# Performance work log

Hardware: AMD Instinct MI355X
Metric: run time of the kernel (lower is better)

## Reference

```python
import jax, jax.numpy as jnp
import numpy as np
import math

D_MODEL = 1024
N_HEADS = 16
D_KV = 64
INNER = N_HEADS * D_KV
NUM_BUCKETS = 32
MAX_DISTANCE = 128


def _relative_position_bucket(relative_position, bidirectional=True,
                              num_buckets=NUM_BUCKETS, max_distance=MAX_DISTANCE):
    # faithful port of T5Attention._relative_position_bucket
    relative_buckets = jnp.zeros_like(relative_position)
    if bidirectional:
        num_buckets //= 2
        relative_buckets = relative_buckets + (relative_position > 0).astype(jnp.int32) * num_buckets
        relative_position = jnp.abs(relative_position)
    else:
        relative_position = -jnp.minimum(relative_position, jnp.zeros_like(relative_position))
    max_exact = num_buckets // 2
    is_small = relative_position < max_exact
    rp_large = max_exact + (
        jnp.log(relative_position.astype(jnp.float32) / max_exact)
        / math.log(max_distance / max_exact) * (num_buckets - max_exact)
    ).astype(jnp.int32)
    rp_large = jnp.minimum(rp_large, num_buckets - 1)
    return relative_buckets + jnp.where(is_small, relative_position, rp_large)


def compute_bias(rel_bias_table, q_len, k_len):
    # [q_len, k_len] relative positions -> bucket ids -> [1, H, q_len, k_len] bias
    context = jnp.arange(q_len, dtype=jnp.int32)[:, None]
    memory = jnp.arange(k_len, dtype=jnp.int32)[None, :]
    buckets = _relative_position_bucket(memory - context, bidirectional=True)
    values = rel_bias_table[buckets]            # [q, k, H]
    return jnp.transpose(values, (2, 0, 1))[None]  # [1, H, q, k]


def setup_inputs() -> dict:
    key = jax.random.key(0)
    ks = jax.random.split(key, 6)
    B, S = 2, 2048
    scale = 0.02
    return {
        "hidden_states": jax.random.normal(ks[0], (B, S, D_MODEL), jnp.float32),
        # weights stored as [in, out] (torch Linear applies x @ W.T with W [out,in])
        "w_q": jax.random.normal(ks[1], (D_MODEL, INNER), jnp.float32) * scale,
        "w_k": jax.random.normal(ks[2], (D_MODEL, INNER), jnp.float32) * scale,
        "w_v": jax.random.normal(ks[3], (D_MODEL, INNER), jnp.float32) * scale,
        "w_o": jax.random.normal(ks[4], (INNER, D_MODEL), jnp.float32) * scale,
        "rel_bias_table": jax.random.normal(ks[5], (NUM_BUCKETS, N_HEADS), jnp.float32) * scale,
    }


def reference(hidden_states, w_q, w_k, w_v, w_o, rel_bias_table):
    B, S, _ = hidden_states.shape

    def shape(x):  # [B, S, inner] -> [B, H, S, d_kv]
        return jnp.transpose(x.reshape(B, S, N_HEADS, D_KV), (0, 2, 1, 3))

    q = shape(hidden_states @ w_q)  # note: T5 applies no 1/sqrt(d) scaling
    k = shape(hidden_states @ w_k)
    v = shape(hidden_states @ w_v)

    scores = jnp.einsum("bhqd,bhkd->bhqk", q, k)
    position_bias = compute_bias(rel_bias_table, S, S)
    scores = scores + position_bias
    attn = jax.nn.softmax(scores.astype(jnp.float32), axis=-1).astype(scores.dtype)
    ctx = jnp.einsum("bhqk,bhkd->bhqd", attn, v)
    ctx = jnp.transpose(ctx, (0, 2, 1, 3)).reshape(B, S, INNER)
    return ctx @ w_o
```

## Files before the change

kernel.cpp:

```cpp
#include <hip/hip_runtime.h>
#include <math.h>

#define S_LEN 2048
#define DM 1024

typedef __attribute__((ext_vector_type(8))) __bf16 bf16x8;
typedef __attribute__((ext_vector_type(4))) float floatx4;

typedef __attribute__((address_space(1))) const unsigned int g_u32;
typedef __attribute__((address_space(3))) unsigned int l_u32;

__device__ __forceinline__ unsigned short f2bf(float f) {
  union { __bf16 h; unsigned short u; } v;
  v.h = (__bf16)f;
  return v.u;
}
__device__ __forceinline__ float bf2f(unsigned short u) {
  union { unsigned int u; float f; } v; v.u = ((unsigned int)u) << 16;
  return v.f;
}
__device__ __forceinline__ bf16x8 ld_frag(const unsigned short* p) {
  union { uint4 u; bf16x8 v; } t;
  t.u = *(const uint4*)p;
  return t.v;
}

__global__ void detect_k(const unsigned short* __restrict__ x, int* __restrict__ flag) {
  __shared__ int cnt;
  if (threadIdx.x == 0) cnt = 0;
  __syncthreads();
  int local = 0;
  for (int i = threadIdx.x; i < 4096; i += 256) {
    unsigned short u = x[i];
    int e = (u >> 7) & 0xFF;
    if (e > 140) local++;
  }
  atomicAdd(&cnt, local);
  __syncthreads();
  if (threadIdx.x == 0) *flag = (cnt > 64) ? 1 : 0;
}

__global__ void prep_k(const void* __restrict__ x, unsigned short* __restrict__ dst,
                       const void* __restrict__ tbl, float* __restrict__ outb,
                       const void* __restrict__ w0, const void* __restrict__ w1,
                       const void* __restrict__ w2, const void* __restrict__ w3,
                       unsigned short* __restrict__ Wcat, unsigned short* __restrict__ Wto,
                       const int* __restrict__ flag) {
  __shared__ float tile[32][33];
  const int bid = blockIdx.x, tid = threadIdx.x;
  if (bid < 2048) {
    int i = bid * 256 + tid;
    if (*flag) {
      const float4* s = (const float4*)x;
      float4 a = s[2 * i], b = s[2 * i + 1];
      union { uint4 u4; unsigned short s[8]; } o;
      o.s[0] = f2bf(a.x); o.s[1] = f2bf(a.y); o.s[2] = f2bf(a.z); o.s[3] = f2bf(a.w);
      o.s[4] = f2bf(b.x); o.s[5] = f2bf(b.y); o.s[6] = f2bf(b.z); o.s[7] = f2bf(b.w);
      ((uint4*)dst)[i] = o.u4;
    } else {
      ((uint4*)dst)[i] = ((const uint4*)x)[i];
    }
  } else if (bid < 2072) {
    int idx = (bid - 2048) * 256 + tid;
    if (idx >= 16 * 384) return;
    int h = idx / 384;
    int j = idx - h * 384;
    int delta = j - 192;
    int bucket = (delta > 0) ? 16 : 0;
    int ad = (delta < 0) ? -delta : delta;
    int smallv;
    if (ad < 8) smallv = ad;
    else {
      int l = (int)(log((double)ad * 0.125) * (8.0 / log(16.0)));
      smallv = 8 + l;
      if (smallv > 15) smallv = 15;
    }
    bucket += smallv;
    float v;
    if (*flag) v = ((const float*)tbl)[bucket * 16 + h];
    else       v = bf2f(((const unsigned short*)tbl)[bucket * 16 + h]);
    outb[idx] = v * 1.44269504f - 24.f;
  } else {
    const int t = bid - 2072;
    const int z = t >> 10, rem = t & 1023;
    const int bx = rem & 31, by = rem >> 5;
    const int tx = tid & 31, ty = tid >> 5;
    const void* src = (z == 0) ? w0 : (z == 1) ? w1 : (z == 2) ? w2 : w3;
    unsigned short* dsty = (z < 3) ? (Wcat + (size_t)z * 1048576) : Wto;
    const int isf = *flag;
    int xc = bx * 32 + tx;
    int y0 = by * 32;
    for (int i = ty; i < 32; i += 8) {
      float v;
      if (isf) v = ((const float*)src)[(size_t)(y0 + i) * DM + xc];
      else     v = bf2f(((const unsigned short*)src)[(size_t)(y0 + i) * DM + xc]);
      tile[i][tx] = v;
    }
    __syncthreads();
    int xo = y0 + tx;
    for (int i = ty; i < 32; i += 8)
      dsty[(size_t)(bx * 32 + i) * DM + xo] = f2bf(tile[tx][i]);
  }
}

__global__ __launch_bounds__(256) void gemm_bt(
    const unsigned short* __restrict__ A, const unsigned short* __restrict__ Bt,
    void* __restrict__ C)
{
  __shared__ __align__(16) unsigned short smem[128 * 136];
  unsigned short* As = smem;
  unsigned short* Bs = smem + 8192;
  const int tid = threadIdx.x;
  const int lane = tid & 63, wave = tid >> 6;
  const int l16 = lane & 15, quad = lane >> 4;
  const int wm = (wave >> 1) << 6, wn = (wave & 1) << 6;
  const int m0 = blockIdx.y << 7, n0 = blockIdx.x << 7;
  const int lrow = lane >> 3, lcol = (lane & 7) << 3;

  floatx4 acc[4][4] = {};

  for (int k0 = 0; k0 < 1024; k0 += 64) {
    __syncthreads();
#pragma unroll
    for (int i = 0; i < 4; ++i) {
      int r0 = wave * 32 + i * 8;
      __builtin_amdgcn_global_load_lds(
          (g_u32*)(const void*)(A + (size_t)(m0 + r0 + lrow) * 1024 + k0 + lcol),
          (l_u32*)(void*)&As[r0 * 64], 16, 0, 0);
      __builtin_amdgcn_global_load_lds(
          (g_u32*)(const void*)(Bt + (size_t)(n0 + r0 + lrow) * 1024 + k0 + lcol),
          (l_u32*)(void*)&Bs[r0 * 64], 16, 0, 0);
    }
    __syncthreads();
#pragma unroll
    for (int ks = 0; ks < 2; ++ks) {
      bf16x8 a[4], b[4];
#pragma unroll
      for (int mi = 0; mi < 4; ++mi)
        a[mi] = *(const bf16x8*)&As[(wm + mi * 16 + l16) * 64 + ks * 32 + quad * 8];
#pragma unroll
      for (int ni = 0; ni < 4; ++ni)
        b[ni] = *(const bf16x8*)&Bs[(wn + ni * 16 + l16) * 64 + ks * 32 + quad * 8];
#pragma unroll
      for (int mi = 0; mi < 4; ++mi)
#pragma unroll
        for (int ni = 0; ni < 4; ++ni)
          acc[mi][ni] = __builtin_amdgcn_mfma_f32_16x16x32_bf16(a[mi], b[ni], acc[mi][ni], 0, 0, 0);
    }
  }

  unsigned short* Cs = (unsigned short*)C;
  const int mat = n0 >> 10;
  if (mat < 2) {
#pragma unroll
    for (int mi = 0; mi < 4; ++mi)
#pragma unroll
      for (int ni = 0; ni < 4; ++ni)
#pragma unroll
        for (int i = 0; i < 4; ++i) {
          int m = m0 + wm + mi * 16 + quad * 4 + i;
          int n = (n0 & 1023) + wn + ni * 16 + l16;
          int b = m >> 11, s = m & 2047, h = n >> 6, d = n & 63;
          Cs[(size_t)mat * 4194304 + (((size_t)(b * 16 + h)) * 2048 + s) * 64 + d] =
              f2bf(acc[mi][ni][i]);
        }
  } else {
    __syncthreads();
#pragma unroll
    for (int mi = 0; mi < 4; ++mi)
#pragma unroll
      for (int ni = 0; ni < 4; ++ni) {
        union { unsigned short s[4]; uint2 u; } w;
#pragma unroll
        for (int i = 0; i < 4; ++i) w.s[i] = f2bf(acc[mi][ni][i]);
        *(uint2*)&smem[(wn + ni * 16 + l16) * 136 + wm + mi * 16 + quad * 4] = w.u;
      }
    __syncthreads();
    const int bb = m0 >> 11, s0 = m0 & 2047, nb = n0 & 1023;
#pragma unroll
    for (int it = 0; it < 8; ++it) {
      int r = it * 16 + (tid >> 4);
      int c = (tid & 15) * 8;
      uint4 rv = *(const uint4*)&smem[r * 136 + c];
      *(uint4*)&Cs[(size_t)2 * 4194304 + (size_t)(bb * 1024 + nb + r) * 2048 + s0 + c] = rv;
    }
  }
}

__global__ __launch_bounds__(256) void gemm_out(
    const unsigned short* __restrict__ A, const unsigned short* __restrict__ Bt,
    void* __restrict__ C, const int* __restrict__ flag)
{
  __shared__ __align__(16) unsigned short As[128 * 64];
  __shared__ __align__(16) unsigned short Bs[64 * 64];
  const int tid = threadIdx.x;
  const int lane = tid & 63, wave = tid >> 6;
  const int l16 = lane & 15, quad = lane >> 4;
  const int wm = (wave >> 1) << 6, wn = (wave & 1) << 5;
  const int m0 = blockIdx.y << 7, n0 = blockIdx.x << 6;
  const int lrow = lane >> 3, lcol = (lane & 7) << 3;

  floatx4 acc[4][2] = {};

  for (int k0 = 0; k0 < 1024; k0 += 64) {
    __syncthreads();
#pragma unroll
    for (int i = 0; i < 4; ++i) {
      int r0 = wave * 32 + i * 8;
      __builtin_amdgcn_global_load_lds(
          (g_u32*)(const void*)(A + (size_t)(m0 + r0 + lrow) * 1024 + k0 + lcol),
          (l_u32*)(void*)&As[r0 * 64], 16, 0, 0);
    }
#pragma unroll
    for (int i = 0; i < 2; ++i) {
      int r0 = wave * 16 + i * 8;
      __builtin_amdgcn_global_load_lds(
          (g_u32*)(const void*)(Bt + (size_t)(n0 + r0 + lrow) * 1024 + k0 + lcol),
          (l_u32*)(void*)&Bs[r0 * 64], 16, 0, 0);
    }
    __syncthreads();
#pragma unroll
    for (int ks = 0; ks < 2; ++ks) {
      bf16x8 a[4], b[2];
#pragma unroll
      for (int mi = 0; mi < 4; ++mi)
        a[mi] = *(const bf16x8*)&As[(wm + mi * 16 + l16) * 64 + ks * 32 + quad * 8];
#pragma unroll
      for (int ni = 0; ni < 2; ++ni)
        b[ni] = *(const bf16x8*)&Bs[(wn + ni * 16 + l16) * 64 + ks * 32 + quad * 8];
#pragma unroll
      for (int mi = 0; mi < 4; ++mi)
#pragma unroll
        for (int ni = 0; ni < 2; ++ni)
          acc[mi][ni] = __builtin_amdgcn_mfma_f32_16x16x32_bf16(a[mi], b[ni], acc[mi][ni], 0, 0, 0);
    }
  }

  const int isf = *flag;
#pragma unroll
  for (int mi = 0; mi < 4; ++mi)
#pragma unroll
    for (int ni = 0; ni < 2; ++ni)
#pragma unroll
      for (int i = 0; i < 4; ++i) {
        int m = m0 + wm + mi * 16 + quad * 4 + i;
        int n = n0 + wn + ni * 16 + l16;
        size_t idx = (size_t)m * 1024 + n;
        float v = acc[mi][ni][i];
        if (isf) ((float*)C)[idx] = v;
        else     ((unsigned short*)C)[idx] = f2bf(v);
      }
}

#define STAGE_KV(kv0, buf)                                                    \
  {                                                                           \
    int rr = tid >> 3;                                                        \
    int sw = ((tid & 7) ^ (rr & 7)) << 3;                                     \
    __builtin_amdgcn_global_load_lds(                                         \
        (g_u32*)(const void*)(Kp + (size_t)((kv0) + rr) * 64 + sw),           \
        (l_u32*)(void*)&Ks[buf][wave * 512], 16, 0, 0);                       \
    __builtin_amdgcn_global_load_lds(                                         \
        (g_u32*)(const void*)(Vp + (size_t)rr * S_LEN + (kv0) + sw),          \
        (l_u32*)(void*)&Vs[buf][wave * 512], 16, 0, 0);                       \
  }

__global__ __launch_bounds__(512, 4) void attn_k(
    const unsigned short* __restrict__ Q, const unsigned short* __restrict__ K,
    const unsigned short* __restrict__ Vt, const float* __restrict__ bias,
    unsigned short* __restrict__ ctx)
{
  __shared__ __align__(16) unsigned short Ks[2][4096];
  __shared__ __align__(16) unsigned short Vs[2][4096];
  __shared__ __align__(16) unsigned short Ps[8][16][72];
  __shared__ float Bls[384];
  const int tid = threadIdx.x;
  const int lane = tid & 63, wave = tid >> 6;
  const int l16 = lane & 15, quad = lane >> 4;
  const int bh = blockIdx.y;
  const int b = bh >> 4, h = bh & 15;
  const int q0 = blockIdx.x << 7;
  const int wq = wave << 4;

  const unsigned short* Qp = Q + (size_t)bh * S_LEN * 64;
  const unsigned short* Kp = K + (size_t)bh * S_LEN * 64;
  const unsigned short* Vp = Vt + (size_t)bh * 64 * S_LEN;
  const float* biasg = bias + h * 384;

  STAGE_KV(0, 0);
  if (tid < 384) Bls[tid] = biasg[tid];

  bf16x8 qf[2];
#pragma unroll
  for (int ks = 0; ks < 2; ++ks)
    qf[ks] = ld_frag(Qp + (size_t)(q0 + wq + l16) * 64 + ks * 32 + quad * 8);

  bf16x8 ones;
  {
    union { unsigned short s[8]; bf16x8 v; } o;
#pragma unroll
    for (int j = 0; j < 8; ++j) o.s[j] = 0x3F80;
    ones = o.v;
  }

  floatx4 oacc[4] = {};
  floatx4 lacc = {};

  const int qwb = q0 + wq;
  const int rbase = 192 + l16 - (quad << 2) - qwb;

  __syncthreads();
  const float Bneg = Bls[0], Bpos = Bls[383];

  for (int kv0 = 0; kv0 < S_LEN; kv0 += 64) {
    const int cur = (kv0 >> 6) & 1;
    if (kv0 + 64 < S_LEN) STAGE_KV(kv0 + 64, cur ^ 1);

    floatx4 sac[4] = {};
#pragma unroll
    for (int ks = 0; ks < 2; ++ks) {
      bf16x8 kf[4];
#pragma unroll
      for (int ni = 0; ni < 4; ++ni)
        kf[ni] = *(const bf16x8*)&Ks[cur][(ni * 16 + l16) * 64 +
                                          ((((ks << 2) + quad) ^ (l16 & 7)) << 3)];
#pragma unroll
      for (int ni = 0; ni < 4; ++ni)
        sac[ni] = __builtin_amdgcn_mfma_f32_16x16x32_bf16(qf[ks], kf[ni], sac[ni], 0, 0, 0);
    }

    {
      const int dmin = kv0 - (qwb + 15);
      const int dmax = kv0 + 63 - qwb;
      if (dmin >= 96 || dmax <= -96) {
        const float bc = (dmin >= 96) ? Bpos : Bneg;
#pragma unroll
        for (int i = 0; i < 4; ++i)
#pragma unroll
          for (int ni = 0; ni < 4; ++ni)
            sac[ni][i] = __builtin_amdgcn_exp2f(fmaf(sac[ni][i], 1.44269504f, bc));
      } else {
#pragma unroll
        for (int i = 0; i < 4; ++i) {
          const int bbase = kv0 + rbase - i;
#pragma unroll
          for (int ni = 0; ni < 4; ++ni)
            sac[ni][i] = __builtin_amdgcn_exp2f(
                fmaf(sac[ni][i], 1.44269504f, Bls[bbase + ni * 16]));
        }
      }
    }

#pragma unroll
    for (int ni = 0; ni < 4; ++ni)
#pragma unroll
      for (int i = 0; i < 4; ++i)
        Ps[wave][quad * 4 + i][ni * 16 + l16] = f2bf(sac[ni][i]);

#pragma unroll
    for (int ks2 = 0; ks2 < 2; ++ks2) {
      bf16x8 af, vf[4];
      af = *(const bf16x8*)&Ps[wave][l16][ks2 * 32 + quad * 8];
#pragma unroll
      for (int ni = 0; ni < 4; ++ni)
        vf[ni] = *(const bf16x8*)&Vs[cur][(ni * 16 + l16) * 64 +
                                          ((((ks2 << 2) + quad) ^ (l16 & 7)) << 3)];
#pragma unroll
      for (int ni = 0; ni < 4; ++ni)
        oacc[ni] = __builtin_amdgcn_mfma_f32_16x16x32_bf16(af, vf[ni], oacc[ni], 0, 0, 0);
      lacc = __builtin_amdgcn_mfma_f32_16x16x32_bf16(af, ones, lacc, 0, 0, 0);
    }

    __syncthreads();
  }

  float linv[4];
#pragma unroll
  for (int i = 0; i < 4; ++i) linv[i] = 1.f / lacc[i];

#pragma unroll
  for (int ni = 0; ni < 4; ++ni)
#pragma unroll
    for (int i = 0; i < 4; ++i) {
      float v = oacc[ni][i] * linv[i];
      int srow = q0 + wq + quad * 4 + i;
      ctx[((size_t)(b * 2048 + srow)) * 1024 + h * 64 + ni * 16 + l16] = f2bf(v);
    }
}

extern "C" void kernel_launch(void* const* d_in, const int* in_sizes, int n_in,
                              void* d_out, int out_size, void* d_ws, size_t ws_size,
                              hipStream_t stream) {
  char* ws = (char*)d_ws;
  unsigned short* Xbf  = (unsigned short*)(ws);
  unsigned short* Wcat = (unsigned short*)(ws + 8388608);
  unsigned short* Wto  = (unsigned short*)(ws + 14680064);
  unsigned short* Qb   = (unsigned short*)(ws + 16777216);
  unsigned short* ctx  = (unsigned short*)(ws + 41943040);
  float*          bias = (float*)(ws + 50331648);
  int*            flag = (int*)(ws + 50593792);

  unsigned short* Kb  = Qb + 4194304;
  unsigned short* Vtb = Qb + 8388608;

  int isf = -1;
  if (in_sizes && n_in > 0) {
    if (in_sizes[0] == 2 * 2048 * 1024 * 4) isf = 1;
    else if (in_sizes[0] == 2 * 2048 * 1024 * 2) isf = 0;
  }
  if (isf < 0)
    detect_k<<<1, 256, 0, stream>>>((const unsigned short*)d_in[0], flag);
  else
    hipMemsetAsync(flag, isf, sizeof(int), stream);

  prep_k<<<6168, 256, 0, stream>>>(d_in[0], Xbf, d_in[5], bias,
                                   d_in[1], d_in[2], d_in[3], d_in[4],
                                   Wcat, Wto, flag);

  gemm_bt<<<dim3(24, 32), 256, 0, stream>>>(Xbf, Wcat, Qb);

  attn_k<<<dim3(16, 32), 512, 0, stream>>>(Qb, Kb, Vtb, bias, ctx);

  gemm_out<<<dim3(16, 32), 256, 0, stream>>>(ctx, Wto, d_out, flag);
}
```

Baseline: 217.3 us.

## Switch attention to 32x32x16 MFMA with 32 query rows per wave

The attention kernel moves from 16x16x32 MFMA tiles to 32x32x16 MFMA, so each wave now handles 32 query rows and each block 256 rows. The grid is halved to 8x32 blocks and launch bounds drop to 2 blocks per CU. This halves K/V LDS traffic per query row and issues fewer, larger MFMAs. In exchange it uses more registers and LDS for P, and launches only 256 blocks, which may leave CUs underfilled.

```diff
diff --git a/kernel.cpp b/kernel.cpp
--- a/kernel.cpp
+++ b/kernel.cpp
@@ -6,6 +6,7 @@
 
 typedef __attribute__((ext_vector_type(8))) __bf16 bf16x8;
 typedef __attribute__((ext_vector_type(4))) float floatx4;
+typedef __attribute__((ext_vector_type(16))) float floatx16;
 
 typedef __attribute__((address_space(1))) const unsigned int g_u32;
 typedef __attribute__((address_space(3))) unsigned int l_u32;
@@ -264,22 +265,22 @@
         (l_u32*)(void*)&Vs[buf][wave * 512], 16, 0, 0);                       \
   }
 
-__global__ __launch_bounds__(512, 4) void attn_k(
+__global__ __launch_bounds__(512, 2) void attn_k(
     const unsigned short* __restrict__ Q, const unsigned short* __restrict__ K,
     const unsigned short* __restrict__ Vt, const float* __restrict__ bias,
     unsigned short* __restrict__ ctx)
 {
   __shared__ __align__(16) unsigned short Ks[2][4096];
   __shared__ __align__(16) unsigned short Vs[2][4096];
-  __shared__ __align__(16) unsigned short Ps[8][16][72];
+  __shared__ __align__(16) unsigned short Ps[8][32][72];
   __shared__ float Bls[384];
   const int tid = threadIdx.x;
   const int lane = tid & 63, wave = tid >> 6;
-  const int l16 = lane & 15, quad = lane >> 4;
+  const int l32 = lane & 31, hi = lane >> 5;
   const int bh = blockIdx.y;
   const int b = bh >> 4, h = bh & 15;
-  const int q0 = blockIdx.x << 7;
-  const int wq = wave << 4;
+  const int q0 = blockIdx.x << 8;
+  const int wq = wave << 5;
 
   const unsigned short* Qp = Q + (size_t)bh * S_LEN * 64;
   const unsigned short* Kp = K + (size_t)bh * S_LEN * 64;
@@ -289,10 +290,11 @@
   STAGE_KV(0, 0);
   if (tid < 384) Bls[tid] = biasg[tid];
 
-  bf16x8 qf[2];
-#pragma unroll
-  for (int ks = 0; ks < 2; ++ks)
-    qf[ks] = ld_frag(Qp + (size_t)(q0 + wq + l16) * 64 + ks * 32 + quad * 8);
+  const int qwb = q0 + wq;
+  bf16x8 qf[4];
+#pragma unroll
+  for (int ks = 0; ks < 4; ++ks)
+    qf[ks] = ld_frag(Qp + (size_t)(qwb + l32) * 64 + ks * 16 + hi * 8);
 
   bf16x8 ones;
   {
@@ -302,11 +304,8 @@
     ones = o.v;
   }
 
-  floatx4 oacc[4] = {};
-  floatx4 lacc = {};
-
-  const int qwb = q0 + wq;
-  const int rbase = 192 + l16 - (quad << 2) - qwb;
+  floatx16 oacc[2] = {};
+  floatx16 lacc = {};
 
   __syncthreads();
   const float Bneg = Bls[0], Bpos = Bls[383];
@@ -315,75 +314,79 @@
     const int cur = (kv0 >> 6) & 1;
     if (kv0 + 64 < S_LEN) STAGE_KV(kv0 + 64, cur ^ 1);
 
-    floatx4 sac[4] = {};
-#pragma unroll
-    for (int ks = 0; ks < 2; ++ks) {
-      bf16x8 kf[4];
-#pragma unroll
-      for (int ni = 0; ni < 4; ++ni)
-        kf[ni] = *(const bf16x8*)&Ks[cur][(ni * 16 + l16) * 64 +
-                                          ((((ks << 2) + quad) ^ (l16 & 7)) << 3)];
-#pragma unroll
-      for (int ni = 0; ni < 4; ++ni)
-        sac[ni] = __builtin_amdgcn_mfma_f32_16x16x32_bf16(qf[ks], kf[ni], sac[ni], 0, 0, 0);
+    floatx16 sac[2] = {};
+#pragma unroll
+    for (int ks = 0; ks < 4; ++ks) {
+      bf16x8 kf[2];
+#pragma unroll
+      for (int blk = 0; blk < 2; ++blk) {
+        int r = blk * 32 + l32;
+        int slot = (ks * 2 + hi) ^ (r & 7);
+        kf[blk] = *(const bf16x8*)&Ks[cur][r * 64 + slot * 8];
+      }
+#pragma unroll
+      for (int blk = 0; blk < 2; ++blk)
+        sac[blk] = __builtin_amdgcn_mfma_f32_32x32x16_bf16(qf[ks], kf[blk], sac[blk], 0, 0, 0);
     }
 
     {
-      const int dmin = kv0 - (qwb + 15);
+      const int dmin = kv0 - (qwb + 31);
       const int dmax = kv0 + 63 - qwb;
       if (dmin >= 96 || dmax <= -96) {
         const float bc = (dmin >= 96) ? Bpos : Bneg;
 #pragma unroll
-        for (int i = 0; i < 4; ++i)
-#pragma unroll
-          for (int ni = 0; ni < 4; ++ni)
-            sac[ni][i] = __builtin_amdgcn_exp2f(fmaf(sac[ni][i], 1.44269504f, bc));
+        for (int blk = 0; blk < 2; ++blk)
+#pragma unroll
+          for (int reg = 0; reg < 16; ++reg)
+            sac[blk][reg] = __builtin_amdgcn_exp2f(fmaf(sac[blk][reg], 1.44269504f, bc));
       } else {
-#pragma unroll
-        for (int i = 0; i < 4; ++i) {
-          const int bbase = kv0 + rbase - i;
-#pragma unroll
-          for (int ni = 0; ni < 4; ++ni)
-            sac[ni][i] = __builtin_amdgcn_exp2f(
-                fmaf(sac[ni][i], 1.44269504f, Bls[bbase + ni * 16]));
-        }
-      }
-    }
-
-#pragma unroll
-    for (int ni = 0; ni < 4; ++ni)
-#pragma unroll
-      for (int i = 0; i < 4; ++i)
-        Ps[wave][quad * 4 + i][ni * 16 + l16] = f2bf(sac[ni][i]);
-
-#pragma unroll
-    for (int ks2 = 0; ks2 < 2; ++ks2) {
-      bf16x8 af, vf[4];
-      af = *(const bf16x8*)&Ps[wave][l16][ks2 * 32 + quad * 8];
-#pragma unroll
-      for (int ni = 0; ni < 4; ++ni)
-        vf[ni] = *(const bf16x8*)&Vs[cur][(ni * 16 + l16) * 64 +
-                                          ((((ks2 << 2) + quad) ^ (l16 & 7)) << 3)];
-#pragma unroll
-      for (int ni = 0; ni < 4; ++ni)
-        oacc[ni] = __builtin_amdgcn_mfma_f32_16x16x32_bf16(af, vf[ni], oacc[ni], 0, 0, 0);
-      lacc = __builtin_amdgcn_mfma_f32_16x16x32_bf16(af, ones, lacc, 0, 0, 0);
-    }
-
-    __syncthreads();
-  }
-
-  float linv[4];
-#pragma unroll
-  for (int i = 0; i < 4; ++i) linv[i] = 1.f / lacc[i];
-
-#pragma unroll
-  for (int ni = 0; ni < 4; ++ni)
-#pragma unroll
-    for (int i = 0; i < 4; ++i) {
-      float v = oacc[ni][i] * linv[i];
-      int srow = q0 + wq + quad * 4 + i;
-      ctx[((size_t)(b * 2048 + srow)) * 1024 + h * 64 + ni * 16 + l16] = f2bf(v);
+        const int base = kv0 + l32 - qwb + 192 - hi * 4;
+#pragma unroll
+        for (int blk = 0; blk < 2; ++blk)
+#pragma unroll
+          for (int reg = 0; reg < 16; ++reg) {
+            const int qroff = (reg & 3) + 8 * (reg >> 2);
+            sac[blk][reg] = __builtin_amdgcn_exp2f(
+                fmaf(sac[blk][reg], 1.44269504f, Bls[base + blk * 32 - qroff]));
+          }
+      }
+    }
+
+#pragma unroll
+    for (int blk = 0; blk < 2; ++blk)
+#pragma unroll
+      for (int reg = 0; reg < 16; ++reg) {
+        int qr = (reg & 3) + 8 * (reg >> 2) + hi * 4;
+        Ps[wave][qr][blk * 32 + l32] = f2bf(sac[blk][reg]);
+      }
+
+#pragma unroll
+    for (int ks = 0; ks < 4; ++ks) {
+      bf16x8 pa = *(const bf16x8*)&Ps[wave][l32][ks * 16 + hi * 8];
+      bf16x8 vf[2];
+#pragma unroll
+      for (int dblk = 0; dblk < 2; ++dblk) {
+        int vr = dblk * 32 + l32;
+        int slot = (ks * 2 + hi) ^ (vr & 7);
+        vf[dblk] = *(const bf16x8*)&Vs[cur][vr * 64 + slot * 8];
+      }
+#pragma unroll
+      for (int dblk = 0; dblk < 2; ++dblk)
+        oacc[dblk] = __builtin_amdgcn_mfma_f32_32x32x16_bf16(pa, vf[dblk], oacc[dblk], 0, 0, 0);
+      lacc = __builtin_amdgcn_mfma_f32_32x32x16_bf16(pa, ones, lacc, 0, 0, 0);
+    }
+
+    __syncthreads();
+  }
+
+#pragma unroll
+  for (int dblk = 0; dblk < 2; ++dblk)
+#pragma unroll
+    for (int reg = 0; reg < 16; ++reg) {
+      float v = oacc[dblk][reg] / lacc[reg];
+      int srow = qwb + (reg & 3) + 8 * (reg >> 2) + hi * 4;
+      int d = dblk * 32 + l32;
+      ctx[((size_t)(b * 2048 + srow)) * 1024 + h * 64 + d] = f2bf(v);
     }
 }
 
@@ -418,7 +421,7 @@
 
   gemm_bt<<<dim3(24, 32), 256, 0, stream>>>(Xbf, Wcat, Qb);
 
-  attn_k<<<dim3(16, 32), 512, 0, stream>>>(Qb, Kb, Vtb, bias, ctx);
+  attn_k<<<dim3(8, 32), 512, 0, stream>>>(Qb, Kb, Vtb, bias, ctx);
 
   gemm_out<<<dim3(16, 32), 256, 0, stream>>>(ctx, Wto, d_out, flag);
 }
```

After: 222.2 us. +2.3%, slower.
